# Kernel optimization log

Hardware: AMD Instinct MI355X
Metric: run time of the kernel (lower is better)

Reference implementation:

```python
import jax, jax.numpy as jnp
from jax import lax
import numpy as np

CH = 16      # channel_n
HID = 128    # update MLP width


def setup_inputs() -> dict:
    key = jax.random.key(0)
    ks = jax.random.split(key, 7)
    B, H, W = 4, 224, 224
    x = jax.random.uniform(ks[0], (B, CH, H, W), dtype=jnp.float32)
    # perception: Conv2d(16 -> 48, 3x3, pad 1, no bias), OIHW
    w_percep = jax.random.normal(ks[1], (CH * 3, CH, 3, 3), jnp.float32) * 0.05
    # update MLP: 1x1 convs == pointwise linears over channels
    w1 = jax.random.normal(ks[2], (HID, CH * 3), jnp.float32) * 0.05
    b1 = jax.random.normal(ks[3], (HID,), jnp.float32) * 0.01
    w2 = jax.random.normal(ks[4], (HID, HID), jnp.float32) * 0.05
    b2 = jax.random.normal(ks[5], (HID,), jnp.float32) * 0.01
    w3 = jax.random.normal(ks[6], (CH, HID), jnp.float32) * 0.05  # no bias
    return {"x": x, "w_percep": w_percep, "w1": w1, "b1": b1,
            "w2": w2, "b2": b2, "w3": w3, "steps": 40}


def reference(x, w_percep, w1, b1, w2, b2, w3, steps):
    dn = ("NCHW", "OIHW", "NCHW")

    def step(x, _):
        # 3x3 perception conv, same padding  -> [B, 48, H, W]
        p = lax.conv_general_dilated(x, w_percep, (1, 1), "SAME",
                                     dimension_numbers=dn)
        # pointwise conv-MLP (1x1 convs as channel einsums)
        h = jax.nn.relu(jnp.einsum("bchw,oc->bohw", p, w1) + b1[None, :, None, None])
        h = jax.nn.relu(jnp.einsum("bchw,oc->bohw", h, w2) + b2[None, :, None, None])
        dx = jnp.einsum("bchw,oc->bohw", h, w3)
        # residual update + clamp to [0, 1] (eval mode: no fire mask)
        return jnp.clip(x + dx, 0.0, 1.0), None

    x, _ = lax.scan(step, x, None, length=steps)
    return x
```

## Files before the change

### kernel.cpp

```cpp
#include <hip/hip_runtime.h>


typedef __attribute__((ext_vector_type(8))) short short8;
typedef __attribute__((ext_vector_type(4))) float float4v;
typedef __attribute__((ext_vector_type(2))) float float2v;
typedef __attribute__((ext_vector_type(2))) unsigned int uint2v;

#define MFMA16(a, b, c) __builtin_amdgcn_mfma_f32_16x16x32_bf16((a), (b), (c), 0, 0, 0)

__device__ __forceinline__ short f2bf(float f) {
  unsigned u = __builtin_bit_cast(unsigned, f);
  return (short)((u + 0x8000u) >> 16);
}

__device__ __forceinline__ unsigned pk2bf(float a, float b) {
#if __has_builtin(__builtin_amdgcn_cvt_pk_bf16_f32)
  typedef __attribute__((ext_vector_type(2))) __bf16 bf2;
  bf2 r = __builtin_amdgcn_cvt_pk_bf16_f32(a, b);
  return __builtin_bit_cast(unsigned, r);
#else
  unsigned ua = __builtin_bit_cast(unsigned, a), ub = __builtin_bit_cast(unsigned, b);
  return ((ua + 0x8000u) >> 16) | (((ub + 0x8000u) >> 16) << 16);
#endif
}

__device__ __forceinline__ void async16(const void* g, void* l) {
  __builtin_amdgcn_global_load_lds((const __attribute__((address_space(1))) void*)g,
                                   (__attribute__((address_space(3))) void*)l,
                                   16, 0, 0);
}

__device__ __forceinline__ void sync_lds() {
  asm volatile("s_waitcnt lgkmcnt(0)\n\ts_barrier" ::: "memory");
}

#define WS_WE    0
#define WS_W2    43008
#define WS_W3    77824
#define WS_B1    82944
#define WS_B2    83456
#define WS_X32A  83968
#define WS_X32B  12929024
#define WS_X16A  25774080
#define WS_X16B  32196608

__global__ void prep_x(const float* __restrict__ x, float* __restrict__ x32,
                       short* __restrict__ x16) {
  int i = blockIdx.x * 256 + threadIdx.x;
  int w = i % 224;
  int h = (i / 224) % 224;
  int c = (i / 50176) & 15;
  int bb = i / 802816;
  float v = x[i];
  int o = ((bb * 224 + h) * 224 + w) * 16 + c;
  x32[o] = v;
  x16[o] = f2bf(v);
}

__global__ void prep_w(const float* __restrict__ wp, const float* __restrict__ w1,
                       const float* __restrict__ b1, const float* __restrict__ w2,
                       const float* __restrict__ b2, const float* __restrict__ w3,
                       short* __restrict__ wE, short* __restrict__ w2t,
                       short* __restrict__ w3t, float* __restrict__ b1p,
                       float* __restrict__ b2p) {
  int i = blockIdx.x * 256 + threadIdx.x;
  if (i < 21504) {
    int o = i / 168, k = i % 168;
    float v = 0.f;
    if (k < 144) {
      int off = k >> 4, c = k & 15;
      for (int c3 = 0; c3 < 48; ++c3)
        v += w1[o * 48 + c3] * wp[c3 * 144 + c * 9 + off];
    }
    wE[i] = f2bf(v);
  } else if (i < 38912) {
    int j = i - 21504;
    int n = j / 136, kk = j % 136;
    float v = 0.f;
    if (kk < 128) { int ch = 16 * (kk & 7) + (kk >> 3); v = w2[n * 128 + ch]; }
    w2t[j] = f2bf(v);
  } else if (i < 41472) {
    int j = i - 38912;
    float v = 0.f;
    if (j < 2176) {
      int n = j / 136, kk = j % 136;
      if (kk < 128) { int ch = 16 * (kk & 7) + (kk >> 3); v = w3[n * 128 + ch]; }
    }
    w3t[j] = f2bf(v);
  } else if (i < 41600) {
    int p = i - 41472;
    b1p[p] = b1[16 * (p & 7) + (p >> 3)];
  } else {
    int p = i - 41600;
    b2p[p] = b2[16 * (p & 7) + (p >> 3)];
  }
}

template <bool LAST>
__global__ __launch_bounds__(512, 4) void ca_step(
    const short* __restrict__ wEg, const short* __restrict__ w2g,
    const short* __restrict__ w3g, const float* __restrict__ b1p,
    const float* __restrict__ b2p, const float* __restrict__ xs32,
    const short* __restrict__ xs16, float* __restrict__ xd32,
    short* __restrict__ xd16, float* __restrict__ dout) {
  __shared__ short sXH[4 * 3616];
  __shared__ short sBUF[2 * 2 * 2176];
  __shared__ short sH2[2 * 2 * 2176];

  const int tid = threadIdx.x;
  const int lane = tid & 63;
  const int wv = tid >> 6;
  const int c16 = lane & 15;
  const int q = lane >> 4;
  const int q8 = q * 8;
  const int qh = q >> 1;
  const int c0 = (q & 1) * 8;

  const int blk = blockIdx.x;
  const int b = blk / 112;
  const int h0 = (blk % 112) * 2;

  const short8 z8 = {0, 0, 0, 0, 0, 0, 0, 0};
  for (int t = wv; t < 28; t += 8) {
    int hr = t / 7, ck = t % 7;
    int hh = h0 - 1 + hr;
    char* l = (char*)sXH + hr * 7232 + 32 + ck * 1024;
    if (hh >= 0 && hh < 224) {
      const char* g = (const char*)xs16 + ((size_t)(b * 224 + hh) * 224) * 32 + ck * 1024;
      async16(g + lane * 16, l);
    } else {
      *(short8*)(l + lane * 16) = z8;
    }
  }
  if (tid < 16) {
    int hr = tid >> 2, wch = tid & 3;
    int colb = (wch < 2) ? 0 : 225;
    *(short8*)((char*)sXH + hr * 7232 + colb * 32 + (wch & 1) * 16) = z8;
  }

  if (wv < 4) {
    const int wq = wv;
    short8 wf[5][2];
#pragma unroll
    for (int kc = 0; kc < 5; ++kc)
#pragma unroll
      for (int n = 0; n < 2; ++n)
        wf[kc][n] = *(const short8*)(wEg + ((2 * wq + n) * 16 + c16) * 168 + kc * 32 + q8);
    const float2v bH = *(const float2v*)(b1p + c16 * 8 + 2 * wq);

    __syncthreads();

    for (int j = 0; j < 16; ++j) {
      if (j < 14) {
        const int t0 = 2 * j, t1 = t0 + 1;
        const int hb0 = ((t0 / 14) * 226 + (t0 % 14) * 16) * 16;
        const int hb1 = ((t1 / 14) * 226 + (t1 % 14) * 16) * 16;
        float4v acc[2][2];
#pragma unroll
        for (int tt = 0; tt < 2; ++tt)
#pragma unroll
          for (int n = 0; n < 2; ++n) acc[tt][n] = (float4v){0.f, 0.f, 0.f, 0.f};
        __builtin_amdgcn_s_setprio(1);
#pragma unroll
        for (int kc = 0; kc < 5; ++kc) {
          int off = kc * 2 + qh;
          if (off > 8) off = 8;
          int dy = (off * 11) >> 5;
          int dxx = off - dy * 3;
          const int ao = (dy * 226 + dxx + c16) * 16 + c0;
          short8 a0 = *(const short8*)(sXH + hb0 + ao);
          short8 a1 = *(const short8*)(sXH + hb1 + ao);
#pragma unroll
          for (int n = 0; n < 2; ++n) {
            acc[0][n] = MFMA16(a0, wf[kc][n], acc[0][n]);
            acc[1][n] = MFMA16(a1, wf[kc][n], acc[1][n]);
          }
        }
        __builtin_amdgcn_s_setprio(0);
#pragma unroll
        for (int tt = 0; tt < 2; ++tt) {
          short* dst = sBUF + ((j & 1) * 2 + tt) * 2176;
#pragma unroll
          for (int r = 0; r < 4; ++r) {
            unsigned d = pk2bf(fmaxf(acc[tt][0][r] + bH[0], 0.f),
                               fmaxf(acc[tt][1][r] + bH[1], 0.f));
            *(unsigned*)(dst + (q * 4 + r) * 136 + c16 * 8 + 2 * wq) = d;
          }
        }
      }
      sync_lds();
    }
  } else {
    const int g = wv - 4;
    short8 w2f[4][2];
    short8 w3f[4];
#pragma unroll
    for (int kc = 0; kc < 4; ++kc)
#pragma unroll
      for (int n = 0; n < 2; ++n)
        w2f[kc][n] = *(const short8*)(w2g + ((2 * g + n) * 16 + c16) * 136 + kc * 32 + q8);
#pragma unroll
    for (int kc = 0; kc < 4; ++kc)
      w3f[kc] = *(const short8*)(w3g + c16 * 136 + kc * 32 + q8);
    const float2v bG = *(const float2v*)(b2p + c16 * 8 + 2 * g);

    __syncthreads();

    for (int j = 0; j < 16; ++j) {
      float4v acc3;
      int cb3 = 0, hglob3 = 0;
      const bool doG3 = (g < 2) && (j >= 2);
      if (doG3) {
        const int t3 = 2 * (j - 2) + g;
        cb3 = (t3 % 14) * 16; hglob3 = h0 + t3 / 14;
        const size_t pix = (size_t)(b * 224 + hglob3) * 224 + cb3 + c16;
        acc3 = *(const float4v*)(xs32 + pix * 16 + q * 4);
      }
      if (j >= 1 && j <= 14) {
        const short* srcA = sBUF + (((j - 1) & 1) * 2 + 0) * 2176;
        const short* srcB = sBUF + (((j - 1) & 1) * 2 + 1) * 2176;
        float4v acc2[2][2];
#pragma unroll
        for (int tt = 0; tt < 2; ++tt)
#pragma unroll
          for (int n = 0; n < 2; ++n) acc2[tt][n] = (float4v){0.f, 0.f, 0.f, 0.f};
        __builtin_amdgcn_s_setprio(1);
#pragma unroll
        for (int kc = 0; kc < 4; ++kc) {
          short8 aA = *(const short8*)(srcA + c16 * 136 + kc * 32 + q8);
          short8 aB = *(const short8*)(srcB + c16 * 136 + kc * 32 + q8);
#pragma unroll
          for (int n = 0; n < 2; ++n) {
            acc2[0][n] = MFMA16(aA, w2f[kc][n], acc2[0][n]);
            acc2[1][n] = MFMA16(aB, w2f[kc][n], acc2[1][n]);
          }
        }
        __builtin_amdgcn_s_setprio(0);
#pragma unroll
        for (int tt = 0; tt < 2; ++tt) {
          short* dsth2 = sH2 + ((j & 1) * 2 + tt) * 2176;
#pragma unroll
          for (int r = 0; r < 4; ++r) {
            unsigned d = pk2bf(fmaxf(acc2[tt][0][r] + bG[0], 0.f),
                               fmaxf(acc2[tt][1][r] + bG[1], 0.f));
            *(unsigned*)(dsth2 + (q * 4 + r) * 136 + c16 * 8 + 2 * g) = d;
          }
        }
      }
      if (doG3) {
        const short* srch2 = sH2 + (((j - 1) & 1) * 2 + g) * 2176;
        __builtin_amdgcn_s_setprio(1);
#pragma unroll
        for (int kc = 0; kc < 4; ++kc) {
          short8 a = *(const short8*)(srch2 + c16 * 136 + kc * 32 + q8);
          acc3 = MFMA16(w3f[kc], a, acc3);
        }
        __builtin_amdgcn_s_setprio(0);
        const size_t pix = (size_t)(b * 224 + hglob3) * 224 + cb3 + c16;
        float4v vv;
#pragma unroll
        for (int r = 0; r < 4; ++r) vv[r] = fminf(fmaxf(acc3[r], 0.f), 1.f);
        if (LAST) {
#pragma unroll
          for (int r = 0; r < 4; ++r)
            dout[((size_t)(b * 16 + q * 4 + r) * 224 + hglob3) * 224 + cb3 + c16] = vv[r];
        } else {
          *(float4v*)(xd32 + pix * 16 + q * 4) = vv;
          *(uint2v*)(xd16 + pix * 16 + q * 4) =
              (uint2v){pk2bf(vv[0], vv[1]), pk2bf(vv[2], vv[3])};
        }
      }
      sync_lds();
    }
  }
}

extern "C" void kernel_launch(void* const* d_in, const int* in_sizes, int n_in,
                              void* d_out, int out_size, void* d_ws, size_t ws_size,
                              hipStream_t stream) {
  const float* x  = (const float*)d_in[0];
  const float* wp = (const float*)d_in[1];
  const float* w1 = (const float*)d_in[2];
  const float* b1 = (const float*)d_in[3];
  const float* w2 = (const float*)d_in[4];
  const float* b2 = (const float*)d_in[5];
  const float* w3 = (const float*)d_in[6];

  char* ws = (char*)d_ws;
  short* wEg = (short*)(ws + WS_WE);
  short* w2g = (short*)(ws + WS_W2);
  short* w3g = (short*)(ws + WS_W3);
  float* b1p = (float*)(ws + WS_B1);
  float* b2p = (float*)(ws + WS_B2);
  float* X32[2] = {(float*)(ws + WS_X32A), (float*)(ws + WS_X32B)};
  short* X16[2] = {(short*)(ws + WS_X16A), (short*)(ws + WS_X16B)};

  prep_x<<<12544, 256, 0, stream>>>(x, X32[0], X16[0]);
  prep_w<<<163, 256, 0, stream>>>(wp, w1, b1, w2, b2, w3, wEg, w2g, w3g, b1p, b2p);

  for (int s = 0; s < 39; ++s) {
    int sb = s & 1;
    ca_step<false><<<448, 512, 0, stream>>>(wEg, w2g, w3g, b1p, b2p,
                                            X32[sb], X16[sb],
                                            X32[1 - sb], X16[1 - sb], nullptr);
  }
  ca_step<true><<<448, 512, 0, stream>>>(wEg, w2g, w3g, b1p, b2p,
                                         X32[1], X16[1],
                                         X32[0], X16[0], (float*)d_out);
}
```

Measured before the change: 1.004 ms.

## Read padded bf16 state directly from global instead of staging halo in LDS

The bf16 state buffer now uses a zero-padded 226x226 layout, cleared once with a memset, so the perception MFMA operands can be loaded straight from global memory with no bounds checks. This removes the async LDS staging of the 4-row halo and the initial block-wide barrier, and shrinks LDS use. Block indices are also swizzled so neighbouring row-pairs go to different slots in launch order, which may change L2 locality. The cost is that each block re-reads overlapping halo rows from global/L2, and the operand loads run at global-memory latency inside the MFMA loop.

After: 1.109 ms. 1.1x slower.

```diff
diff --git a/kernel.cpp b/kernel.cpp
--- a/kernel.cpp
+++ b/kernel.cpp
@@ -24,12 +24,6 @@
 #endif
 }
 
-__device__ __forceinline__ void async16(const void* g, void* l) {
-  __builtin_amdgcn_global_load_lds((const __attribute__((address_space(1))) void*)g,
-                                   (__attribute__((address_space(3))) void*)l,
-                                   16, 0, 0);
-}
-
 __device__ __forceinline__ void sync_lds() {
   asm volatile("s_waitcnt lgkmcnt(0)\n\ts_barrier" ::: "memory");
 }
@@ -42,7 +36,8 @@
 #define WS_X32A  83968
 #define WS_X32B  12929024
 #define WS_X16A  25774080
-#define WS_X16B  32196608
+#define WS_X16B  32311808
+#define X16_BYTES 6537728
 
 __global__ void prep_x(const float* __restrict__ x, float* __restrict__ x32,
                        short* __restrict__ x16) {
@@ -52,9 +47,8 @@
   int c = (i / 50176) & 15;
   int bb = i / 802816;
   float v = x[i];
-  int o = ((bb * 224 + h) * 224 + w) * 16 + c;
-  x32[o] = v;
-  x16[o] = f2bf(v);
+  x32[((bb * 224 + h) * 224 + w) * 16 + c] = v;
+  x16[((bb * 226 + h + 1) * 226 + (w + 1)) * 16 + c] = f2bf(v);
 }
 
 __global__ void prep_w(const float* __restrict__ wp, const float* __restrict__ w1,
@@ -103,7 +97,6 @@
     const float* __restrict__ b2p, const float* __restrict__ xs32,
     const short* __restrict__ xs16, float* __restrict__ xd32,
     short* __restrict__ xd16, float* __restrict__ dout) {
-  __shared__ short sXH[4 * 3616];
   __shared__ short sBUF[2 * 2 * 2176];
   __shared__ short sH2[2 * 2 * 2176];
 
@@ -114,29 +107,10 @@
   const int q = lane >> 4;
   const int q8 = q * 8;
   const int qh = q >> 1;
-  const int c0 = (q & 1) * 8;
-
-  const int blk = blockIdx.x;
+
+  const int blk = (blockIdx.x & 7) * 56 + (blockIdx.x >> 3);
   const int b = blk / 112;
   const int h0 = (blk % 112) * 2;
-
-  const short8 z8 = {0, 0, 0, 0, 0, 0, 0, 0};
-  for (int t = wv; t < 28; t += 8) {
-    int hr = t / 7, ck = t % 7;
-    int hh = h0 - 1 + hr;
-    char* l = (char*)sXH + hr * 7232 + 32 + ck * 1024;
-    if (hh >= 0 && hh < 224) {
-      const char* g = (const char*)xs16 + ((size_t)(b * 224 + hh) * 224) * 32 + ck * 1024;
-      async16(g + lane * 16, l);
-    } else {
-      *(short8*)(l + lane * 16) = z8;
-    }
-  }
-  if (tid < 16) {
-    int hr = tid >> 2, wch = tid & 3;
-    int colb = (wch < 2) ? 0 : 225;
-    *(short8*)((char*)sXH + hr * 7232 + colb * 32 + (wch & 1) * 16) = z8;
-  }
 
   if (wv < 4) {
     const int wq = wv;
@@ -148,13 +122,23 @@
         wf[kc][n] = *(const short8*)(wEg + ((2 * wq + n) * 16 + c16) * 168 + kc * 32 + q8);
     const float2v bH = *(const float2v*)(b1p + c16 * 8 + 2 * wq);
 
-    __syncthreads();
+    const short* xb = xs16 + (size_t)b * 226 * 226 * 16;
+    int prel[5];
+#pragma unroll
+    for (int kc = 0; kc < 5; ++kc) {
+      int off = kc * 2 + qh;
+      if (off > 8) off = 8;
+      int dy = (off * 11) >> 5;
+      int dxx = off - dy * 3;
+      prel[kc] = (dy * 226 + dxx) * 16;
+    }
+    const int laneoff = c16 * 16 + (q & 1) * 8;
 
     for (int j = 0; j < 16; ++j) {
       if (j < 14) {
         const int t0 = 2 * j, t1 = t0 + 1;
-        const int hb0 = ((t0 / 14) * 226 + (t0 % 14) * 16) * 16;
-        const int hb1 = ((t1 / 14) * 226 + (t1 % 14) * 16) * 16;
+        const short* p0 = xb + ((h0 + t0 / 14) * 226 + (t0 % 14) * 16) * 16 + laneoff;
+        const short* p1 = xb + ((h0 + t1 / 14) * 226 + (t1 % 14) * 16) * 16 + laneoff;
         float4v acc[2][2];
 #pragma unroll
         for (int tt = 0; tt < 2; ++tt)
@@ -163,13 +147,8 @@
         __builtin_amdgcn_s_setprio(1);
 #pragma unroll
         for (int kc = 0; kc < 5; ++kc) {
-          int off = kc * 2 + qh;
-          if (off > 8) off = 8;
-          int dy = (off * 11) >> 5;
-          int dxx = off - dy * 3;
-          const int ao = (dy * 226 + dxx + c16) * 16 + c0;
-          short8 a0 = *(const short8*)(sXH + hb0 + ao);
-          short8 a1 = *(const short8*)(sXH + hb1 + ao);
+          short8 a0 = *(const short8*)(p0 + prel[kc]);
+          short8 a1 = *(const short8*)(p1 + prel[kc]);
 #pragma unroll
           for (int n = 0; n < 2; ++n) {
             acc[0][n] = MFMA16(a0, wf[kc][n], acc[0][n]);
@@ -203,8 +182,6 @@
     for (int kc = 0; kc < 4; ++kc)
       w3f[kc] = *(const short8*)(w3g + c16 * 136 + kc * 32 + q8);
     const float2v bG = *(const float2v*)(b2p + c16 * 8 + 2 * g);
-
-    __syncthreads();
 
     for (int j = 0; j < 16; ++j) {
       float4v acc3;
@@ -256,7 +233,6 @@
           acc3 = MFMA16(w3f[kc], a, acc3);
         }
         __builtin_amdgcn_s_setprio(0);
-        const size_t pix = (size_t)(b * 224 + hglob3) * 224 + cb3 + c16;
         float4v vv;
 #pragma unroll
         for (int r = 0; r < 4; ++r) vv[r] = fminf(fmaxf(acc3[r], 0.f), 1.f);
@@ -265,8 +241,10 @@
           for (int r = 0; r < 4; ++r)
             dout[((size_t)(b * 16 + q * 4 + r) * 224 + hglob3) * 224 + cb3 + c16] = vv[r];
         } else {
+          const size_t pix = (size_t)(b * 224 + hglob3) * 224 + cb3 + c16;
           *(float4v*)(xd32 + pix * 16 + q * 4) = vv;
-          *(uint2v*)(xd16 + pix * 16 + q * 4) =
+          const size_t pp = ((size_t)(b * 226 + hglob3 + 1)) * 226 + cb3 + 1 + c16;
+          *(uint2v*)(xd16 + pp * 16 + q * 4) =
               (uint2v){pk2bf(vv[0], vv[1]), pk2bf(vv[2], vv[3])};
         }
       }
@@ -295,6 +273,7 @@
   float* X32[2] = {(float*)(ws + WS_X32A), (float*)(ws + WS_X32B)};
   short* X16[2] = {(short*)(ws + WS_X16A), (short*)(ws + WS_X16B)};
 
+  hipMemsetAsync(ws + WS_X16A, 0, 2 * (size_t)X16_BYTES, stream);
   prep_x<<<12544, 256, 0, stream>>>(x, X32[0], X16[0]);
   prep_w<<<163, 256, 0, stream>>>(wp, w1, b1, w2, b2, w3, wEg, w2g, w3g, b1p, b2p);
 
```
